# Kernel tuning notes

Hardware: AMD Instinct MI355X
Metric: run time of the kernel (lower is better)

The kernel has to match this reference:

```python
import jax, jax.numpy as jnp
import numpy as np

SIGMA = 1.0
S = 1.0 / (2.0 * SIGMA * SIGMA)  # 0.5


def setup_inputs() -> dict:
    key = jax.random.key(0)
    k1, k2 = jax.random.split(key)
    inputs = jax.random.normal(k1, (32, 4096, 3), dtype=jnp.float32)  # (B, N, D) point cloud
    # stars initialized RandomUniform(-1, 1) in the original build()
    stars = jax.random.uniform(k2, (1024, 3), minval=-1.0, maxval=1.0, dtype=jnp.float32)  # (M, D)
    return {"inputs": inputs, "stars": stars}


def reference(inputs, stars):
    # out[b, m] = sum_n exp(-S * ||inputs[b, n] - stars[m]||^2)
    # Use ||a-b||^2 = ||a||^2 - 2 a.b + ||b||^2 to avoid the (B, M, N, D) diff tensor.
    x2 = jnp.sum(inputs * inputs, axis=-1)          # (B, N)
    s2 = jnp.sum(stars * stars, axis=-1)            # (M,)
    cross = jnp.einsum('bnd,md->bmn', inputs, stars)  # (B, M, N)
    d2 = x2[:, None, :] - 2.0 * cross + s2[None, :, None]  # (B, M, N)
    return jnp.sum(jnp.exp(-S * d2), axis=2)        # (B, M)
```

## Files before the change

kernel.cpp:

```cpp
#include <hip/hip_runtime.h>


typedef float f32x2 __attribute__((ext_vector_type(2)));

#define NB 32
#define NN 4096
#define NM 1024
#define NCHUNK 32
#define NPB (NN / NCHUNK)
#define NPAIR (NPB / 2)
#define TPB 256
#define MPT (NM / TPB)

__device__ __forceinline__ float exp2_hw(float x) {
    float r;
    asm("v_exp_f32 %0, %1" : "=v"(r) : "v"(x));
    return r;
}

__device__ __forceinline__ f32x2 pk_fma(f32x2 a, f32x2 b, f32x2 c) {
    f32x2 d;
    asm("v_pk_fma_f32 %0, %1, %2, %3" : "=v"(d) : "v"(a), "v"(b), "v"(c));
    return d;
}

__global__ __launch_bounds__(TPB, 4) void gau_part(const float* __restrict__ inputs,
                                                   const float* __restrict__ stars,
                                                   float* __restrict__ part) {
    constexpr float C2  = 0.72134752044448169f;
    constexpr float L2E = 1.44269504088896340f;

    const int b     = blockIdx.x / NCHUNK;
    const int chunk = blockIdx.x % NCHUNK;
    const int t     = threadIdx.x;

    f32x2 Sx2[MPT], Sy2[MPT], Sz2[MPT], K2[MPT], acc[MPT];
#pragma unroll
    for (int k = 0; k < MPT; ++k) {
        int m = t + k * TPB;
        float sx = stars[3 * m + 0];
        float sy = stars[3 * m + 1];
        float sz = stars[3 * m + 2];
        float a = L2E * sx, c = L2E * sy, e = L2E * sz;
        float kk = -C2 * (sx * sx + sy * sy + sz * sz);
        Sx2[k] = f32x2{a, a};
        Sy2[k] = f32x2{c, c};
        Sz2[k] = f32x2{e, e};
        K2[k]  = f32x2{kk, kk};
        acc[k] = f32x2{0.0f, 0.0f};
    }

    const float* pp = inputs + ((size_t)b * NN + (size_t)chunk * NPB) * 3;

#pragma unroll 4
    for (int i = 0; i < NPAIR; ++i) {
        float x0 = pp[6 * i + 0], y0 = pp[6 * i + 1], z0 = pp[6 * i + 2];
        float x1 = pp[6 * i + 3], y1 = pp[6 * i + 4], z1 = pp[6 * i + 5];
        float q0 = -C2 * x0 * x0 - C2 * y0 * y0 - C2 * z0 * z0;
        float q1 = -C2 * x1 * x1 - C2 * y1 * y1 - C2 * z1 * z1;
        f32x2 E2 = f32x2{exp2_hw(q0), exp2_hw(q1)};
        f32x2 x2 = f32x2{x0, x1};
        f32x2 y2 = f32x2{y0, y1};
        f32x2 z2 = f32x2{z0, z1};
#pragma unroll
        for (int k = 0; k < MPT; ++k) {
            f32x2 inner = pk_fma(Sx2[k], x2, pk_fma(Sy2[k], y2, pk_fma(Sz2[k], z2, K2[k])));
            f32x2 e2 = f32x2{exp2_hw(inner.x), exp2_hw(inner.y)};
            acc[k] = pk_fma(E2, e2, acc[k]);
        }
    }

    float* pb = part + ((size_t)b * NCHUNK + chunk) * NM;
#pragma unroll
    for (int k = 0; k < MPT; ++k) {
        pb[t + k * TPB] = acc[k].x + acc[k].y;
    }
}

__global__ __launch_bounds__(256) void gau_reduce(const float* __restrict__ part,
                                                  float* __restrict__ out) {
    const int o = blockIdx.x * 256 + threadIdx.x;
    const int b = o >> 10;
    const int m = o & (NM - 1);
    const float* pb = part + (size_t)b * NCHUNK * NM + m;
    float s = 0.0f;
#pragma unroll
    for (int c = 0; c < NCHUNK; ++c) {
        s += pb[(size_t)c * NM];
    }
    out[o] = s;
}

extern "C" void kernel_launch(void* const* d_in, const int* in_sizes, int n_in,
                              void* d_out, int out_size, void* d_ws, size_t ws_size,
                              hipStream_t stream) {
    const float* inputs = (const float*)d_in[0];
    const float* stars  = (const float*)d_in[1];
    float* out  = (float*)d_out;
    float* part = (float*)d_ws;

    gau_part<<<NB * NCHUNK, TPB, 0, stream>>>(inputs, stars, part);
    gau_reduce<<<(NB * NM) / 256, 256, 0, stream>>>(part, out);
}
```

Before: 34.06 us.

## Broadcast points via readlane from per-lane loads and drop packed FMA

Each lane now loads one point and computes its self-Gaussian term once, then points are broadcast to the wave with readlane, so the per-iteration uniform global loads and redundant exp of the point norm go away. Packed FMA pairs are replaced by scalar FMAs. The chunk count doubles to 64 points per block and occupancy hint rises to 8 blocks per CU. The partial-sum buffer and reduce kernel now handle twice as many chunks, and scalar FMAs may cost more VALU issue than the packed form.

```diff
diff --git a/kernel.cpp b/kernel.cpp
--- a/kernel.cpp
+++ b/kernel.cpp
@@ -1,14 +1,11 @@
 #include <hip/hip_runtime.h>
 
-
-typedef float f32x2 __attribute__((ext_vector_type(2)));
 
 #define NB 32
 #define NN 4096
 #define NM 1024
-#define NCHUNK 32
+#define NCHUNK 64
 #define NPB (NN / NCHUNK)
-#define NPAIR (NPB / 2)
 #define TPB 256
 #define MPT (NM / TPB)
 
@@ -18,13 +15,11 @@
     return r;
 }
 
-__device__ __forceinline__ f32x2 pk_fma(f32x2 a, f32x2 b, f32x2 c) {
-    f32x2 d;
-    asm("v_pk_fma_f32 %0, %1, %2, %3" : "=v"(d) : "v"(a), "v"(b), "v"(c));
-    return d;
+__device__ __forceinline__ float bcast(float v, int j) {
+    return __int_as_float(__builtin_amdgcn_readlane(__float_as_int(v), j));
 }
 
-__global__ __launch_bounds__(TPB, 4) void gau_part(const float* __restrict__ inputs,
+__global__ __launch_bounds__(TPB, 8) void gau_part(const float* __restrict__ inputs,
                                                    const float* __restrict__ stars,
                                                    float* __restrict__ part) {
     constexpr float C2  = 0.72134752044448169f;
@@ -33,47 +28,45 @@
     const int b     = blockIdx.x / NCHUNK;
     const int chunk = blockIdx.x % NCHUNK;
     const int t     = threadIdx.x;
+    const int lane  = t & 63;
 
-    f32x2 Sx2[MPT], Sy2[MPT], Sz2[MPT], K2[MPT], acc[MPT];
+    float Sx[MPT], Sy[MPT], Sz[MPT], K[MPT], acc[MPT];
 #pragma unroll
     for (int k = 0; k < MPT; ++k) {
         int m = t + k * TPB;
         float sx = stars[3 * m + 0];
         float sy = stars[3 * m + 1];
         float sz = stars[3 * m + 2];
-        float a = L2E * sx, c = L2E * sy, e = L2E * sz;
-        float kk = -C2 * (sx * sx + sy * sy + sz * sz);
-        Sx2[k] = f32x2{a, a};
-        Sy2[k] = f32x2{c, c};
-        Sz2[k] = f32x2{e, e};
-        K2[k]  = f32x2{kk, kk};
-        acc[k] = f32x2{0.0f, 0.0f};
+        Sx[k] = L2E * sx;
+        Sy[k] = L2E * sy;
+        Sz[k] = L2E * sz;
+        K[k]  = -C2 * (sx * sx + sy * sy + sz * sz);
+        acc[k] = 0.0f;
     }
 
-    const float* pp = inputs + ((size_t)b * NN + (size_t)chunk * NPB) * 3;
+    const float* p = inputs + ((size_t)b * NN + (size_t)chunk * NPB + lane) * 3;
+    float px = p[0], py = p[1], pz = p[2];
+    float pE = exp2_hw(-C2 * px * px - C2 * py * py - C2 * pz * pz);
 
-#pragma unroll 4
-    for (int i = 0; i < NPAIR; ++i) {
-        float x0 = pp[6 * i + 0], y0 = pp[6 * i + 1], z0 = pp[6 * i + 2];
-        float x1 = pp[6 * i + 3], y1 = pp[6 * i + 4], z1 = pp[6 * i + 5];
-        float q0 = -C2 * x0 * x0 - C2 * y0 * y0 - C2 * z0 * z0;
-        float q1 = -C2 * x1 * x1 - C2 * y1 * y1 - C2 * z1 * z1;
-        f32x2 E2 = f32x2{exp2_hw(q0), exp2_hw(q1)};
-        f32x2 x2 = f32x2{x0, x1};
-        f32x2 y2 = f32x2{y0, y1};
-        f32x2 z2 = f32x2{z0, z1};
+#pragma unroll 8
+    for (int j = 0; j < 64; ++j) {
+        float x = bcast(px, j);
+        float y = bcast(py, j);
+        float z = bcast(pz, j);
+        float E = bcast(pE, j);
 #pragma unroll
         for (int k = 0; k < MPT; ++k) {
-            f32x2 inner = pk_fma(Sx2[k], x2, pk_fma(Sy2[k], y2, pk_fma(Sz2[k], z2, K2[k])));
-            f32x2 e2 = f32x2{exp2_hw(inner.x), exp2_hw(inner.y)};
-            acc[k] = pk_fma(E2, e2, acc[k]);
+            float u = fmaf(z, Sz[k], K[k]);
+            u = fmaf(y, Sy[k], u);
+            u = fmaf(x, Sx[k], u);
+            acc[k] = fmaf(E, exp2_hw(u), acc[k]);
         }
     }
 
     float* pb = part + ((size_t)b * NCHUNK + chunk) * NM;
 #pragma unroll
     for (int k = 0; k < MPT; ++k) {
-        pb[t + k * TPB] = acc[k].x + acc[k].y;
+        pb[t + k * TPB] = acc[k];
     }
 }
 
```

Measured after the change: 39.55 us. 1.16x slower.
